# Performance work log

Measured on AMD Instinct MI355X. Metric: run time of the kernel, lower is better.

The kernel has to match this reference:

```python
import jax, jax.numpy as jnp
import numpy as np

B, N, T, H, F = 2, 1024, 12, 64, 1

def _diffuse(x, a):
    # x: (B,C,V), a: (B,W,V)  ->  (B,C,W)   (einsum 'ncvl,nwv->ncwl' with l=1)
    return jnp.einsum('bcv,bwv->bcw', x, a)

def _sconv(x, supports, order, include_self, W, b):
    feats = [x] if include_self else []
    for a in supports:
        x1 = _diffuse(x, a)
        feats.append(x1)
        for _ in range(order - 1):
            x1 = _diffuse(x1, a)
            feats.append(x1)
    z = jnp.concatenate(feats, axis=1)
    return jnp.einsum('bcn,oc->bon', z, W) + b[None, :, None]

def _lin(x, W, b):
    # Conv1d/Conv2d with kernel 1 == channel-wise linear
    return jnp.einsum('bcn,oc->bon', x, W) + b[None, :, None]

def setup_inputs():
    key = jax.random.key(0)
    ks = jax.random.split(key, 12)
    x = jax.random.normal(ks[0], (B, F, N, T), jnp.float32)
    mask = jax.random.randint(ks[1], (B, F, N, T), 0, 2, jnp.int32)
    adj = jax.random.uniform(ks[2], (2, B, N, N), jnp.float32)
    adj = adj / (adj.sum(-1, keepdims=True) + 1e-8)  # compute_support row-normalization
    cin_gate = 5 * (2 * F + H)  # (order*support_len+1)*(d_in+num_units) = 5*66
    s = 0.1
    Wr = s * jax.random.normal(ks[3], (H, cin_gate)); br = jnp.zeros((H,), jnp.float32)
    Wu = s * jax.random.normal(ks[4], (H, cin_gate)); bu = jnp.zeros((H,), jnp.float32)
    Wc = s * jax.random.normal(ks[5], (H, cin_gate)); bc = jnp.zeros((H,), jnp.float32)
    Wfs = s * jax.random.normal(ks[6], (F, H)); bfs = jnp.zeros((F,), jnp.float32)
    Wdin = s * jax.random.normal(ks[7], (H, 2 * F + H)); bdin = jnp.zeros((H,), jnp.float32)
    Wgc = s * jax.random.normal(ks[8], (H, 2 * H)); bgc = jnp.zeros((H,), jnp.float32)
    Wlout = s * jax.random.normal(ks[9], (H, 2 * H)); blout = jnp.zeros((H,), jnp.float32)
    Wro = s * jax.random.normal(ks[10], (F, 2 * H)); bro = jnp.zeros((F,), jnp.float32)
    prelu_a = 0.25 * jnp.ones((1,), jnp.float32)
    return dict(x=x, mask=mask, adj=adj, Wr=Wr, br=br, Wu=Wu, bu=bu, Wc=Wc, bc=bc,
                Wfs=Wfs, bfs=bfs, Wdin=Wdin, bdin=bdin, Wgc=Wgc, bgc=bgc,
                Wlout=Wlout, blout=blout, Wro=Wro, bro=bro, prelu_a=prelu_a)

def _gril(x, mask, adj, Wr, br, Wu, bu, Wc, bc, Wfs, bfs, Wdin, bdin,
          Wgc, bgc, Wlout, blout, Wro, bro, prelu_a):
    supports = [adj[0], adj[1]]
    h0 = jnp.zeros((x.shape[0], H, x.shape[2]), x.dtype)

    def step(h, inp):
        x_s, m_s = inp                  # (B,F,N), (B,F,N) int
        m_f = m_s.astype(x_s.dtype)
        m_b = m_s.astype(bool)
        # first stage prediction from hidden state
        xs1 = _lin(h, Wfs, bfs)
        x1 = jnp.where(m_b, x_s, xs1)
        # spatial decoder (order=1, no attention)
        x_in = _lin(jnp.concatenate([x1, m_f, h], axis=1), Wdin, bdin)
        out = _sconv(x_in, supports, 1, False, Wgc, bgc)
        out = _lin(jnp.concatenate([out, h], axis=1), Wlout, blout)
        out = jnp.where(out >= 0, out, prelu_a * out)   # PReLU
        repr_s = jnp.concatenate([out, h], axis=1)      # (B,2H,N)
        xs2 = _lin(repr_s, Wro, bro)
        x2 = jnp.where(m_b, x1, xs2)
        # GCGRU cell update (order=2 diffusion per gate)
        inp_c = jnp.concatenate([x2, m_f], axis=1)
        xh = jnp.concatenate([inp_c, h], axis=1)
        r = jax.nn.sigmoid(_sconv(xh, supports, 2, True, Wr, br))
        u = jax.nn.sigmoid(_sconv(xh, supports, 2, True, Wu, bu))
        xc = jnp.concatenate([inp_c, r * h], axis=1)
        c = jnp.tanh(_sconv(xc, supports, 2, True, Wc, bc))
        h_new = u * h + (1.0 - u) * c
        return h_new, (xs2, xs1, repr_s)

    xs = jnp.moveaxis(x, -1, 0)     # (T,B,F,N)
    ms = jnp.moveaxis(mask, -1, 0)
    _, (imps, preds, reprs) = jax.lax.scan(step, h0, (xs, ms))
    imputations = jnp.moveaxis(imps, 0, -1)       # (B,F,N,T)
    predictions = jnp.moveaxis(preds, 0, -1)      # (B,F,N,T)
    representations = jnp.moveaxis(reprs, 0, -1)  # (B,2H,N,T)
    return imputations, predictions, representations

def reference(x, mask, adj, Wr, br, Wu, bu, Wc, bc, Wfs, bfs, Wdin, bdin,
              Wgc, bgc, Wlout, blout, Wro, bro, prelu_a):
    return _gril(x, mask, adj, Wr, br, Wu, bu, Wc, bc, Wfs, bfs, Wdin, bdin,
                 Wgc, bgc, Wlout, blout, Wro, bro, prelu_a)
```

## Files before the change

### kernel.cpp

```cpp
#include <hip/hip_runtime.h>
#include <hip/hip_bf16.h>
#include <cstddef>

#define NN 1024
#define BB 2
#define TT 12
#define ZS 352

typedef __attribute__((ext_vector_type(8))) short short8;
typedef __attribute__((ext_vector_type(4))) short short4v;
typedef __attribute__((ext_vector_type(4))) float f32x4;
typedef __hip_bfloat16 bf16;

__device__ __forceinline__ float sigmoidf_(float v) { return 1.0f / (1.0f + expf(-v)); }
__device__ __forceinline__ short bf16s(float f) { bf16 h = __float2bfloat16(f); return *reinterpret_cast<short*>(&h); }

__device__ __forceinline__ float mapcol(const float* src, int c) {
    if (c < 64) return src[2 + c];
    if (c == 64) return src[0];
    if (c == 65) return src[1];
    if (c < 68 || c >= 340) return 0.f;
    const int d = c - 68, bk = d / 68, off = d % 68;
    if (off < 64) return src[66 + bk * 66 + 2 + off];
    if (off == 64) return src[66 + bk * 66];
    if (off == 65) return src[66 + bk * 66 + 1];
    return 0.f;
}

__global__ __launch_bounds__(256) void k_prep(
    const float* __restrict__ Wgc, const float* __restrict__ bgc,
    const float* __restrict__ Wdin, const float* __restrict__ bdin,
    const float* __restrict__ Wlout, const float* __restrict__ blout,
    const float* __restrict__ Wfs,
    const float* __restrict__ Wr, const float* __restrict__ Wu, const float* __restrict__ Wc,
    float* __restrict__ Wcomb, float* __restrict__ bcomb, float* __restrict__ blout2,
    bf16* __restrict__ Wpre, bf16* __restrict__ Wrub, bf16* __restrict__ Wcb,
    bf16* __restrict__ Wlb)
{
    const int idx = blockIdx.x * 256 + threadIdx.x;
    if (idx < 8448) {
        const int o = idx / 66, k = idx % 66;
        const float* g = Wgc + (size_t)(o & 63) * 128 + (o >> 6) * 64;
        float a = 0.f;
#pragma unroll 8
        for (int c = 0; c < 64; ++c) a += g[c] * Wdin[c * 66 + k];
        Wcomb[idx] = a;
    } else if (idx < 8576) {
        const int o = idx - 8448;
        const float* g = Wgc + (size_t)(o & 63) * 128 + (o >> 6) * 64;
        float a = 0.f;
#pragma unroll 8
        for (int c = 0; c < 64; ++c) a += g[c] * bdin[c];
        bcomb[o] = a;
    } else if (idx < 8640) {
        const int oc = idx - 8576;
        float a = blout[oc];
#pragma unroll 8
        for (int j = 0; j < 64; ++j) a += Wlout[(size_t)oc * 128 + j] * bgc[j];
        blout2[oc] = a;
    } else if (idx < 17856) {
        const int j = idx - 8640, r = j >> 6, k = j & 63;
        float v = 0.f;
        if (r == 0) v = Wfs[k];
        else if (r <= 128) {
            const int o = r - 1;
            const float* g = Wgc + (size_t)(o & 63) * 128 + (o >> 6) * 64;
#pragma unroll 8
            for (int c = 0; c < 64; ++c) v += g[c] * Wdin[c * 66 + 2 + k];
        }
        Wpre[j] = __float2bfloat16(v);
    } else if (idx < 62912) {
        const int j = idx - 17856, r = j / 352, c = j % 352;
        const float* src = (r < 64) ? (Wr + (size_t)r * 330) : (Wu + (size_t)(r - 64) * 330);
        Wrub[j] = __float2bfloat16(mapcol(src, c));
    } else if (idx < 85440) {
        const int j = idx - 62912, r = j / 352, c = j % 352;
        Wcb[j] = __float2bfloat16(mapcol(Wc + (size_t)r * 330, c));
    } else if (idx < 93632) {
        const int j = idx - 85440;
        Wlb[j] = __float2bfloat16(Wlout[j]);
    }
}

__global__ __launch_bounds__(256) void k_cvtT(const float* __restrict__ adj,
                                              bf16* __restrict__ adjb, bf16* __restrict__ adjtb)
{
    const int sb = blockIdx.z;
    const int r0 = blockIdx.y * 64, c0 = blockIdx.x * 64;
    const float* A = adj + ((size_t)sb << 20);
    __shared__ short tile[64][72];
    const int tr = threadIdx.x >> 4, tc = (threadIdx.x & 15) * 4;
#pragma unroll
    for (int i = 0; i < 4; ++i) {
        const int r = tr + i * 16;
        float4 v = *reinterpret_cast<const float4*>(&A[(size_t)(r0 + r) * NN + c0 + tc]);
        short4v o = { bf16s(v.x), bf16s(v.y), bf16s(v.z), bf16s(v.w) };
        *reinterpret_cast<short4v*>(&adjb[((size_t)sb << 20) + (size_t)(r0 + r) * NN + c0 + tc]) = o;
        tile[r][tc + 0] = o.x; tile[r][tc + 1] = o.y; tile[r][tc + 2] = o.z; tile[r][tc + 3] = o.w;
    }
    __syncthreads();
#pragma unroll
    for (int i = 0; i < 4; ++i) {
        const int v = tr + i * 16;
        short4v o = { tile[tc + 0][v], tile[tc + 1][v], tile[tc + 2][v], tile[tc + 3][v] };
        *reinterpret_cast<short4v*>(&adjtb[((size_t)sb << 20) + (size_t)(c0 + v) * NN + r0 + tc]) = o;
    }
}

__global__ __launch_bounds__(256) void k_a2(const bf16* __restrict__ adjb,
                                            const bf16* __restrict__ adjtb,
                                            bf16* __restrict__ adj2b)
{
    const int sb = blockIdx.z;
    const int wave = threadIdx.x >> 6, lane = threadIdx.x & 63;
    const int lr = lane & 15, lq = lane >> 4;
    const int v0 = blockIdx.x * 128 + wave * 32;
    const int w0 = blockIdx.y * 64;
    const bf16* AT = adjtb + ((size_t)sb << 20) + (size_t)(v0 + lr) * NN + lq * 8;
    const bf16* Ar = adjb + ((size_t)sb << 20) + (size_t)(w0 + lr) * NN + lq * 8;
    f32x4 acc[4][2];
#pragma unroll
    for (int m = 0; m < 4; ++m)
#pragma unroll
        for (int nb = 0; nb < 2; ++nb) acc[m][nb] = (f32x4){0.f, 0.f, 0.f, 0.f};
#pragma unroll 2
    for (int k0 = 0; k0 < NN; k0 += 32) {
        short8 bfr[2], af[4];
#pragma unroll
        for (int nb = 0; nb < 2; ++nb)
            bfr[nb] = *reinterpret_cast<const short8*>(AT + (size_t)nb * 16 * NN + k0);
#pragma unroll
        for (int m = 0; m < 4; ++m)
            af[m] = *reinterpret_cast<const short8*>(Ar + (size_t)m * 16 * NN + k0);
#pragma unroll
        for (int m = 0; m < 4; ++m)
#pragma unroll
            for (int nb = 0; nb < 2; ++nb)
                acc[m][nb] = __builtin_amdgcn_mfma_f32_16x16x32_bf16(af[m], bfr[nb], acc[m][nb], 0, 0, 0);
    }
    bf16* D = adj2b + ((size_t)sb << 20);
#pragma unroll
    for (int m = 0; m < 4; ++m)
#pragma unroll
        for (int nb = 0; nb < 2; ++nb)
#pragma unroll
            for (int q = 0; q < 4; ++q)
                D[(size_t)(w0 + m * 16 + lq * 4 + q) * NN + v0 + nb * 16 + lr] = __float2bfloat16(acc[m][nb][q]);
}

__global__ __launch_bounds__(64) void k_pre(
    const bf16* __restrict__ Wpre, const bf16* __restrict__ zT,
    const float* __restrict__ Wcomb, const float* __restrict__ bcomb,
    const float* __restrict__ bfsp,
    const float* __restrict__ x, const int* __restrict__ mask,
    bf16* __restrict__ yb, float* __restrict__ pred, int t)
{
    const int lane = threadIdx.x & 63, lr = lane & 15, lq = lane >> 4;
    const int p = blockIdx.x * 16 + lr;
    const bf16* B = zT + (size_t)p * ZS;
    f32x4 acc[9];
#pragma unroll
    for (int m = 0; m < 9; ++m) acc[m] = (f32x4){0.f, 0.f, 0.f, 0.f};
#pragma unroll
    for (int ks = 0; ks < 2; ++ks) {
        short8 bfr = *reinterpret_cast<const short8*>(B + ks * 32 + lq * 8);
#pragma unroll
        for (int m = 0; m < 9; ++m) {
            short8 af = *reinterpret_cast<const short8*>(Wpre + (size_t)(m * 16 + lr) * 64 + ks * 32 + lq * 8);
            acc[m] = __builtin_amdgcn_mfma_f32_16x16x32_bf16(af, bfr, acc[m], 0, 0, 0);
        }
    }
    const int b = p >> 10, n = p & (NN - 1);
    const size_t xi = (size_t)p * TT + t;
    const float xs1v = acc[0][0] + bfsp[0];
    const float xs1 = __shfl(xs1v, lr);
    const int mi = mask[xi];
    const float mf = (float)mi;
    const float x1 = mi ? x[xi] : xs1;
    if (lq == 0) pred[xi] = xs1;
#pragma unroll
    for (int m = 0; m < 9; ++m)
#pragma unroll
        for (int q = 0; q < 4; ++q) {
            const int o = m * 16 + lq * 4 + q - 1;
            if (o >= 0 && o < 128) {
                const float val = acc[m][q] + Wcomb[o * 66] * x1 + Wcomb[o * 66 + 1] * mf + bcomb[o];
                yb[(size_t)(b * 128 + o) * NN + n] = __float2bfloat16(val);
            }
        }
}

__global__ __launch_bounds__(256) void k_difA(
    const bf16* __restrict__ adjb, const bf16* __restrict__ adj2b,
    const bf16* __restrict__ yb, const bf16* __restrict__ zbi,
    const bf16* __restrict__ Wlb, const float* __restrict__ blout2,
    const float* __restrict__ prelu_a, const float* __restrict__ Wro,
    const float* __restrict__ bro, const float* __restrict__ x,
    const int* __restrict__ mask, const float* __restrict__ hTf,
    float* __restrict__ imp, float* __restrict__ repr,
    bf16* __restrict__ zb, bf16* __restrict__ zcb,
    bf16* __restrict__ zT, bf16* __restrict__ zcT, int t)
{
    const int wave = threadIdx.x >> 6, lane = threadIdx.x & 63;
    const int lr = lane & 15, lq = lane >> 4;
    const int n0 = blockIdx.x * 32;

    __shared__ f32x4 red[3][2][2][4][64];
    __shared__ short gh[32][136];
    __shared__ float hf[32][68];
    __shared__ float lo_sm[32][68];

    if (blockIdx.y >= 2) {
        const int i = blockIdx.y - 2;
        const int b = i & 1, s = (i >> 1) & 1, ord = i >> 2;
        const int sb = s * 2 + b;
        const bf16* M = (ord ? adj2b : adjb) + ((size_t)sb << 20);
        const bf16* A = M + (size_t)(n0 + lr) * NN + lq * 8;
        const bf16* Xp = zbi + ((size_t)(b * 66 + lr)) * NN + lq * 8;
        f32x4 acc[2][4];
#pragma unroll
        for (int nt = 0; nt < 2; ++nt)
#pragma unroll
            for (int m = 0; m < 4; ++m) acc[nt][m] = (f32x4){0.f, 0.f, 0.f, 0.f};
        const int vbeg = wave * 256;
#pragma unroll 2
        for (int it = 0; it < 8; ++it) {
            const int v0 = vbeg + it * 32;
            short8 bfr[2], af[4];
#pragma unroll
            for (int nt = 0; nt < 2; ++nt)
                bfr[nt] = *reinterpret_cast<const short8*>(A + (size_t)nt * 16 * NN + v0);
#pragma unroll
            for (int m = 0; m < 4; ++m)
                af[m] = *reinterpret_cast<const short8*>(Xp + (size_t)m * 16 * NN + v0);
#pragma unroll
            for (int nt = 0; nt < 2; ++nt)
#pragma unroll
                for (int m = 0; m < 4; ++m)
                    acc[nt][m] = __builtin_amdgcn_mfma_f32_16x16x32_bf16(af[m], bfr[nt], acc[nt][m], 0, 0, 0);
        }
        if (wave > 0) {
#pragma unroll
            for (int nt = 0; nt < 2; ++nt)
#pragma unroll
                for (int m = 0; m < 4; ++m) red[wave - 1][0][nt][m][lane] = acc[nt][m];
        }
        __syncthreads();
        if (wave == 0) {
#pragma unroll
            for (int nt = 0; nt < 2; ++nt) {
#pragma unroll
                for (int m = 0; m < 4; ++m)
                    acc[nt][m] += red[0][0][nt][m][lane] + red[1][0][nt][m][lane] + red[2][0][nt][m][lane];
                const int p = b * NN + n0 + nt * 16 + lr;
                bf16* dst = zT + (size_t)p * ZS + 68 + (s * 2 + ord) * 68;
#pragma unroll
                for (int m = 0; m < 4; ++m) {
                    short4v o = { bf16s(acc[nt][m][0]), bf16s(acc[nt][m][1]),
                                  bf16s(acc[nt][m][2]), bf16s(acc[nt][m][3]) };
                    *reinterpret_cast<short4v*>(dst + m * 16 + lq * 4) = o;
                }
            }
        }
        return;
    }

    const int b = blockIdx.y;
    f32x4 acc[2][2][4];
#pragma unroll
    for (int s = 0; s < 2; ++s)
#pragma unroll
        for (int nt = 0; nt < 2; ++nt)
#pragma unroll
            for (int m = 0; m < 4; ++m) acc[s][nt][m] = (f32x4){0.f, 0.f, 0.f, 0.f};
    {
        const int vbeg = wave * 256;
#pragma unroll 2
        for (int it = 0; it < 8; ++it) {
            const int v0 = vbeg + it * 32;
            short8 bfr[2][2], af[2][4];
#pragma unroll
            for (int s = 0; s < 2; ++s) {
                const bf16* M = adjb + ((size_t)(s * 2 + b) << 20);
#pragma unroll
                for (int nt = 0; nt < 2; ++nt)
                    bfr[s][nt] = *reinterpret_cast<const short8*>(M + (size_t)(n0 + nt * 16 + lr) * NN + v0 + lq * 8);
#pragma unroll
                for (int m = 0; m < 4; ++m)
                    af[s][m] = *reinterpret_cast<const short8*>(yb + (size_t)(b * 128 + s * 64 + m * 16 + lr) * NN + v0 + lq * 8);
            }
#pragma unroll
            for (int s = 0; s < 2; ++s)
#pragma unroll
                for (int nt = 0; nt < 2; ++nt)
#pragma unroll
                    for (int m = 0; m < 4; ++m)
                        acc[s][nt][m] = __builtin_amdgcn_mfma_f32_16x16x32_bf16(af[s][m], bfr[s][nt], acc[s][nt][m], 0, 0, 0);
        }
    }
    if (wave > 0) {
#pragma unroll
        for (int s = 0; s < 2; ++s)
#pragma unroll
            for (int nt = 0; nt < 2; ++nt)
#pragma unroll
                for (int m = 0; m < 4; ++m) red[wave - 1][s][nt][m][lane] = acc[s][nt][m];
    }
    if (wave == 1 || wave == 2) {
        const int nb = (wave - 1) * 16;
        for (int i = lane; i < 1024; i += 64) {
            const int node = nb + (i >> 6), oc = i & 63;
            const float hv = hTf[(size_t)(b * NN + n0 + node) * 64 + oc];
            hf[node][oc] = hv;
            gh[node][64 + oc] = bf16s(hv);
            repr[(((size_t)b * 128 + 64 + oc) * NN + (n0 + node)) * TT + t] = hv;
        }
    }
    __syncthreads();
    if (wave == 0) {
#pragma unroll
        for (int nt = 0; nt < 2; ++nt) {
#pragma unroll
            for (int m = 0; m < 4; ++m) {
                f32x4 g = acc[0][nt][m] + acc[1][nt][m];
#pragma unroll
                for (int w = 0; w < 3; ++w) g += red[w][0][nt][m][lane] + red[w][1][nt][m][lane];
                const int node = nt * 16 + lr;
#pragma unroll
                for (int q = 0; q < 4; ++q) gh[node][m * 16 + lq * 4 + q] = bf16s(g[q]);
            }
        }
    }
    __syncthreads();
    {
        f32x4 dacc[2];
#pragma unroll
        for (int nt = 0; nt < 2; ++nt) dacc[nt] = (f32x4){0.f, 0.f, 0.f, 0.f};
#pragma unroll
        for (int ks = 0; ks < 4; ++ks) {
            short8 af = *reinterpret_cast<const short8*>(Wlb + (size_t)(wave * 16 + lr) * 128 + ks * 32 + lq * 8);
#pragma unroll
            for (int nt = 0; nt < 2; ++nt) {
                short8 bfr = *reinterpret_cast<const short8*>(&gh[nt * 16 + lr][ks * 32 + lq * 8]);
                dacc[nt] = __builtin_amdgcn_mfma_f32_16x16x32_bf16(af, bfr, dacc[nt], 0, 0, 0);
            }
        }
        const float pa = prelu_a[0];
#pragma unroll
        for (int nt = 0; nt < 2; ++nt) {
            const int node = nt * 16 + lr;
#pragma unroll
            for (int q = 0; q < 4; ++q) {
                const int oc = wave * 16 + lq * 4 + q;
                float v = dacc[nt][q] + blout2[oc];
                v = (v >= 0.f) ? v : pa * v;
                repr[(((size_t)b * 128 + oc) * NN + (n0 + node)) * TT + t] = v;
                lo_sm[node][oc] = v;
            }
        }
    }
    __syncthreads();
    {
        const int node = threadIdx.x >> 3, sub = threadIdx.x & 7;
        float s = 0.f;
#pragma unroll
        for (int j = sub * 8; j < sub * 8 + 8; ++j)
            s += Wro[j] * lo_sm[node][j] + Wro[64 + j] * hf[node][j];
        s += __shfl_xor(s, 1); s += __shfl_xor(s, 2); s += __shfl_xor(s, 4);
        if (sub == 0) {
            const float xs2 = s + bro[0];
            const int n = n0 + node;
            const int p = b * NN + n;
            const size_t xi = (size_t)p * TT + t;
            imp[xi] = xs2;
            const int mi = mask[xi];
            const float x2 = mi ? x[xi] : xs2;
            const bf16 x2b = __float2bfloat16(x2);
            const bf16 mb = __float2bfloat16((float)mi);
            zb[((size_t)b * 66 + 64) * NN + n] = x2b;
            zb[((size_t)b * 66 + 65) * NN + n] = mb;
            zcb[((size_t)b * 66 + 64) * NN + n] = x2b;
            zcb[((size_t)b * 66 + 65) * NN + n] = mb;
            zT[(size_t)p * ZS + 64] = x2b; zT[(size_t)p * ZS + 65] = mb;
            zcT[(size_t)p * ZS + 64] = x2b; zcT[(size_t)p * ZS + 65] = mb;
        }
    }
}

__global__ __launch_bounds__(256) void k_difN(
    const bf16* __restrict__ adjb, const bf16* __restrict__ adj2b,
    const bf16* __restrict__ zcb, float* __restrict__ gcT_unused,
    bf16* __restrict__ zcT)
{
    const int i = blockIdx.y;
    const int b = i & 1, s = (i >> 1) & 1, ord = i >> 2;
    const int wave = threadIdx.x >> 6, lane = threadIdx.x & 63;
    const int lr = lane & 15, lq = lane >> 4;
    const int n0 = blockIdx.x * 32;
    const int sb = s * 2 + b;
    const bf16* M = (ord ? adj2b : adjb) + ((size_t)sb << 20);
    const bf16* A = M + (size_t)(n0 + lr) * NN + lq * 8;
    const bf16* Xp = zcb + ((size_t)(b * 66 + lr)) * NN + lq * 8;

    f32x4 acc[2][4];
#pragma unroll
    for (int nt = 0; nt < 2; ++nt)
#pragma unroll
        for (int m = 0; m < 4; ++m) acc[nt][m] = (f32x4){0.f, 0.f, 0.f, 0.f};
    const int vbeg = wave * 256;
#pragma unroll 2
    for (int it = 0; it < 8; ++it) {
        const int v0 = vbeg + it * 32;
        short8 bfr[2], af[4];
#pragma unroll
        for (int nt = 0; nt < 2; ++nt)
            bfr[nt] = *reinterpret_cast<const short8*>(A + (size_t)nt * 16 * NN + v0);
#pragma unroll
        for (int m = 0; m < 4; ++m)
            af[m] = *reinterpret_cast<const short8*>(Xp + (size_t)m * 16 * NN + v0);
#pragma unroll
        for (int nt = 0; nt < 2; ++nt)
#pragma unroll
            for (int m = 0; m < 4; ++m)
                acc[nt][m] = __builtin_amdgcn_mfma_f32_16x16x32_bf16(af[m], bfr[nt], acc[nt][m], 0, 0, 0);
    }
    __shared__ f32x4 red[3][2][4][64];
    if (wave > 0) {
#pragma unroll
        for (int nt = 0; nt < 2; ++nt)
#pragma unroll
            for (int m = 0; m < 4; ++m) red[wave - 1][nt][m][lane] = acc[nt][m];
    }
    __syncthreads();
    if (wave == 0) {
#pragma unroll
        for (int nt = 0; nt < 2; ++nt) {
#pragma unroll
            for (int m = 0; m < 4; ++m)
                acc[nt][m] += red[0][nt][m][lane] + red[1][nt][m][lane] + red[2][nt][m][lane];
            const int p = b * NN + n0 + nt * 16 + lr;
            bf16* dst = zcT + (size_t)p * ZS + 68 + (s * 2 + ord) * 68;
#pragma unroll
            for (int m = 0; m < 4; ++m) {
                short4v o = { bf16s(acc[nt][m][0]), bf16s(acc[nt][m][1]),
                              bf16s(acc[nt][m][2]), bf16s(acc[nt][m][3]) };
                *reinterpret_cast<short4v*>(dst + m * 16 + lq * 4) = o;
            }
        }
    }
}

__global__ __launch_bounds__(256) void k_dif2(
    const bf16* __restrict__ adjb, const bf16* __restrict__ adj2b,
    const bf16* __restrict__ zb, bf16* __restrict__ zT, bf16* __restrict__ zcT)
{
    const int i = blockIdx.y;
    const int b = i & 1, s = (i >> 1) & 1, ord = i >> 2;
    const int sb = s * 2 + b;
    const int wave = threadIdx.x >> 6, lane = threadIdx.x & 63;
    const int lr = lane & 15, lq = lane >> 4;
    const int n0 = blockIdx.x * 16;
    const bf16* M = (ord ? adj2b : adjb) + ((size_t)sb << 20);
    const bf16* A = M + (size_t)(n0 + lr) * NN + lq * 8;
    const bf16* Xp = zb + ((size_t)(b * 66 + 64) + lr) * NN + lq * 8;

    f32x4 acc = (f32x4){0.f, 0.f, 0.f, 0.f};
    const short8 zsh = {0, 0, 0, 0, 0, 0, 0, 0};
    const int vbeg = wave * 256;
#pragma unroll 4
    for (int i2 = 0; i2 < 8; ++i2) {
        const int v0 = vbeg + i2 * 32;
        short8 bfr = *reinterpret_cast<const short8*>(A + v0);
        short8 af = (lr < 2) ? *reinterpret_cast<const short8*>(Xp + v0) : zsh;
        acc = __builtin_amdgcn_mfma_f32_16x16x32_bf16(af, bfr, acc, 0, 0, 0);
    }
    __shared__ f32x4 red2[3][64];
    if (wave > 0) red2[wave - 1][lane] = acc;
    __syncthreads();
    if (wave == 0 && lq == 0) {
        acc += red2[0][lane] + red2[1][lane] + red2[2][lane];
        const int p = b * NN + n0 + lr;
        const size_t off = (size_t)p * ZS + 68 + (s * 2 + ord) * 68 + 64;
#pragma unroll
        for (int q = 0; q < 2; ++q) {
            const bf16 v = __float2bfloat16(acc[q]);
            zT[off + q] = v; zcT[off + q] = v;
        }
    }
}

__global__ __launch_bounds__(128) void k_gates(
    const bf16* __restrict__ Wrub, const bf16* __restrict__ zT,
    const float* __restrict__ br, const float* __restrict__ bu,
    const float* __restrict__ hTf,
    float* __restrict__ uT, bf16* __restrict__ zcb, bf16* __restrict__ zcT)
{
    const int wave = threadIdx.x >> 6, lane = threadIdx.x & 63;
    const int lr = lane & 15, lq = lane >> 4;
    const int p = blockIdx.x * 16 + lr;
    const bf16* B = zT + (size_t)p * ZS;
    const bf16* WA = Wrub + (size_t)wave * 64 * ZS;
    f32x4 acc[4];
#pragma unroll
    for (int m = 0; m < 4; ++m) acc[m] = (f32x4){0.f, 0.f, 0.f, 0.f};
#pragma unroll 2
    for (int ks = 0; ks < 11; ++ks) {
        short8 bfr = *reinterpret_cast<const short8*>(B + ks * 32 + lq * 8);
#pragma unroll
        for (int m = 0; m < 4; ++m) {
            short8 af = *reinterpret_cast<const short8*>(WA + (size_t)(m * 16 + lr) * ZS + ks * 32 + lq * 8);
            acc[m] = __builtin_amdgcn_mfma_f32_16x16x32_bf16(af, bfr, acc[m], 0, 0, 0);
        }
    }
    const int b = p >> 10, n = p & (NN - 1);
    if (wave == 0) {
#pragma unroll
        for (int m = 0; m < 4; ++m) {
            short4v rq;
#pragma unroll
            for (int q = 0; q < 4; ++q) {
                const int oc = m * 16 + lq * 4 + q;
                const float rv = sigmoidf_(acc[m][q] + br[oc]);
                const float rh = rv * hTf[(size_t)p * 64 + oc];
                rq[q] = bf16s(rh);
                zcb[((size_t)b * 66 + oc) * NN + n] = __float2bfloat16(rh);
            }
            *reinterpret_cast<short4v*>(&zcT[(size_t)p * ZS + m * 16 + lq * 4]) = rq;
        }
    } else {
#pragma unroll
        for (int m = 0; m < 4; ++m) {
            f32x4 uq;
#pragma unroll
            for (int q = 0; q < 4; ++q) {
                const int oc = m * 16 + lq * 4 + q;
                uq[q] = sigmoidf_(acc[m][q] + bu[oc]);
            }
            *reinterpret_cast<f32x4*>(&uT[(size_t)p * 64 + m * 16 + lq * 4]) = uq;
        }
    }
}

__global__ __launch_bounds__(128) void k_cellpre(
    const bf16* __restrict__ Wcb, const bf16* __restrict__ zcT,
    const float* __restrict__ bc, const float* __restrict__ uT,
    float* __restrict__ hTf, bf16* __restrict__ zT, bf16* __restrict__ zb,
    const bf16* __restrict__ Wpre, const float* __restrict__ Wcomb,
    const float* __restrict__ bcomb, const float* __restrict__ bfsp,
    const float* __restrict__ x, const int* __restrict__ mask,
    bf16* __restrict__ yb, float* __restrict__ pred, int tn)
{
    const int wave = threadIdx.x >> 6, lane = threadIdx.x & 63;
    const int lr = lane & 15, lq = lane >> 4;
    const int p = blockIdx.x * 16 + lr;
    const int b = p >> 10, n = p & (NN - 1);
    __shared__ short hsm[16][72];
    __shared__ float xs1s[16];

    {
        const bf16* B = zcT + (size_t)p * ZS;
        f32x4 acc[2];
#pragma unroll
        for (int mm = 0; mm < 2; ++mm) acc[mm] = (f32x4){0.f, 0.f, 0.f, 0.f};
#pragma unroll 2
        for (int ks = 0; ks < 11; ++ks) {
            short8 bfr = *reinterpret_cast<const short8*>(B + ks * 32 + lq * 8);
#pragma unroll
            for (int mm = 0; mm < 2; ++mm) {
                const int m = wave * 2 + mm;
                short8 af = *reinterpret_cast<const short8*>(Wcb + (size_t)(m * 16 + lr) * ZS + ks * 32 + lq * 8);
                acc[mm] = __builtin_amdgcn_mfma_f32_16x16x32_bf16(af, bfr, acc[mm], 0, 0, 0);
            }
        }
#pragma unroll
        for (int mm = 0; mm < 2; ++mm) {
            const int m = wave * 2 + mm;
            f32x4 hq;
            short4v hb;
#pragma unroll
            for (int q = 0; q < 4; ++q) {
                const int oc = m * 16 + lq * 4 + q;
                const float cv = tanhf(acc[mm][q] + bc[oc]);
                const float uv = uT[(size_t)p * 64 + oc];
                const float ho = hTf[(size_t)p * 64 + oc];
                const float hn = uv * ho + (1.f - uv) * cv;
                hq[q] = hn;
                hb[q] = bf16s(hn);
                zb[((size_t)b * 66 + oc) * NN + n] = __float2bfloat16(hn);
            }
            *reinterpret_cast<f32x4*>(&hTf[(size_t)p * 64 + m * 16 + lq * 4]) = hq;
            *reinterpret_cast<short4v*>(&zT[(size_t)p * ZS + m * 16 + lq * 4]) = hb;
            *reinterpret_cast<short4v*>(&hsm[lr][m * 16 + lq * 4]) = hb;
        }
    }
    __syncthreads();

    {
        const int MB = wave ? 4 : 5;
        f32x4 acc[5];
#pragma unroll
        for (int m = 0; m < 5; ++m) acc[m] = (f32x4){0.f, 0.f, 0.f, 0.f};
#pragma unroll
        for (int ks = 0; ks < 2; ++ks) {
            short8 bfr = *reinterpret_cast<const short8*>(&hsm[lr][ks * 32 + lq * 8]);
#pragma unroll
            for (int m = 0; m < 5; ++m) {
                if (m < MB) {
                    const int mm = wave ? 5 + m : m;
                    short8 af = *reinterpret_cast<const short8*>(Wpre + (size_t)(mm * 16 + lr) * 64 + ks * 32 + lq * 8);
                    acc[m] = __builtin_amdgcn_mfma_f32_16x16x32_bf16(af, bfr, acc[m], 0, 0, 0);
                }
            }
        }
        if (wave == 0 && lq == 0) xs1s[lr] = acc[0][0] + bfsp[0];
        __syncthreads();
        const float xs1 = xs1s[lr];
        const size_t xi = (size_t)p * TT + tn;
        const int mi = mask[xi];
        const float mf = (float)mi;
        const float x1 = mi ? x[xi] : xs1;
        if (wave == 0 && lq == 0) pred[xi] = xs1;
#pragma unroll
        for (int m = 0; m < 5; ++m) {
            if (m < MB) {
                const int mm = wave ? 5 + m : m;
#pragma unroll
                for (int q = 0; q < 4; ++q) {
                    const int o = mm * 16 + lq * 4 + q - 1;
                    if (o >= 0 && o < 128) {
                        const float val = acc[m][q] + Wcomb[o * 66] * x1 + Wcomb[o * 66 + 1] * mf + bcomb[o];
                        yb[(size_t)(b * 128 + o) * NN + n] = __float2bfloat16(val);
                    }
                }
            }
        }
    }
}

extern "C" void kernel_launch(void* const* d_in, const int* in_sizes, int n_in,
                              void* d_out, int out_size, void* d_ws, size_t ws_size,
                              hipStream_t stream)
{
    const float* x     = (const float*)d_in[0];
    const int*   mask  = (const int*)  d_in[1];
    const float* adj   = (const float*)d_in[2];
    const float* Wr    = (const float*)d_in[3];
    const float* br    = (const float*)d_in[4];
    const float* Wu    = (const float*)d_in[5];
    const float* bu    = (const float*)d_in[6];
    const float* Wc    = (const float*)d_in[7];
    const float* bc    = (const float*)d_in[8];
    const float* Wfs   = (const float*)d_in[9];
    const float* bfs   = (const float*)d_in[10];
    const float* Wdin  = (const float*)d_in[11];
    const float* bdin  = (const float*)d_in[12];
    const float* Wgc   = (const float*)d_in[13];
    const float* bgc   = (const float*)d_in[14];
    const float* Wlout = (const float*)d_in[15];
    const float* blout = (const float*)d_in[16];
    const float* Wro   = (const float*)d_in[17];
    const float* bro   = (const float*)d_in[18];
    const float* pa    = (const float*)d_in[19];

    float* ws = (float*)d_ws;
    float* Wcomb  = ws + 0;
    float* bcomb  = ws + 8448;
    float* blout2 = ws + 8576;
    float* uT     = ws + 272832;
    float* hTf    = ws + 403904;
    bf16* bfp   = (bf16*)(ws + 534976);
    bf16* zb    = bfp + 0;
    bf16* zcb   = bfp + 135168;
    bf16* zT    = bfp + 270336;
    bf16* zcT   = bfp + 991232;
    bf16* adjb  = bfp + 1712128;
    bf16* adjtb = bfp + 5906432;
    bf16* adj2b = bfp + 10100736;
    bf16* yb    = bfp + 14295040;
    bf16* Wpre  = bfp + 14557184;
    bf16* Wrub  = bfp + 14566400;
    bf16* Wcb   = bfp + 14611456;
    bf16* Wlb   = bfp + 14633984;

    float* imp  = (float*)d_out;
    float* pred = imp + (size_t)BB * NN * TT;
    float* repr = imp + (size_t)2 * BB * NN * TT;

    hipMemsetAsync(hTf, 0, 131072 * 4 + (size_t)1712128 * 2, stream);
    hipLaunchKernelGGL(k_prep, dim3(366), dim3(256), 0, stream,
                       Wgc, bgc, Wdin, bdin, Wlout, blout, Wfs, Wr, Wu, Wc,
                       Wcomb, bcomb, blout2, Wpre, Wrub, Wcb, Wlb);
    hipLaunchKernelGGL(k_cvtT, dim3(16, 16, 4), dim3(256), 0, stream, adj, adjb, adjtb);
    hipLaunchKernelGGL(k_a2, dim3(8, 16, 4), dim3(256), 0, stream, adjb, adjtb, adj2b);

    hipLaunchKernelGGL(k_pre, dim3(128), dim3(64), 0, stream,
                       Wpre, zT, Wcomb, bcomb, bfs, x, mask, yb, pred, 0);

    for (int t = 0; t < TT; ++t) {
        const int ny = (t < TT - 1) ? 10 : 2;
        hipLaunchKernelGGL(k_difA, dim3(32, ny), dim3(256), 0, stream,
                           adjb, adj2b, yb, zb, Wlb, blout2, pa, Wro, bro, x, mask,
                           hTf, imp, repr, zb, zcb, zT, zcT, t);
        if (t < TT - 1) {
            hipLaunchKernelGGL(k_dif2, dim3(64, 8), dim3(256), 0, stream,
                               adjb, adj2b, zb, zT, zcT);
            hipLaunchKernelGGL(k_gates, dim3(128), dim3(128), 0, stream,
                               Wrub, zT, br, bu, hTf, uT, zcb, zcT);
            hipLaunchKernelGGL(k_difN, dim3(32, 8), dim3(256), 0, stream,
                               adjb, adj2b, zcb, (float*)nullptr, zcT);
            hipLaunchKernelGGL(k_cellpre, dim3(128), dim3(128), 0, stream,
                               Wcb, zcT, bc, uT, hTf, zT, zb,
                               Wpre, Wcomb, bcomb, bfs, x, mask, yb, pred, t + 1);
        }
    }
}
```

Measured before the change: 705.0 us.

## Fuse input-channel diffusion into gates kernel and apply it as fp32 rank-8 correction

Removes the separate k_dif2 launch that diffused the two input channels (x2, mask) and wrote them into zT/zcT. The gates kernel now runs those diffusions on two extra waves alongside the MFMA gate GEMM. The results are applied as an fp32 rank-8 correction using weights split out of Wr/Wu/Wc, and are stored to a buffer so the cell kernel can reuse them. This saves one launch per timestep and keeps those columns in fp32, at the cost of a larger block in k_gates and extra scalar correction math.

```diff
diff --git a/kernel.cpp b/kernel.cpp
--- a/kernel.cpp
+++ b/kernel.cpp
@@ -15,15 +15,13 @@
 __device__ __forceinline__ float sigmoidf_(float v) { return 1.0f / (1.0f + expf(-v)); }
 __device__ __forceinline__ short bf16s(float f) { bf16 h = __float2bfloat16(f); return *reinterpret_cast<short*>(&h); }
 
-__device__ __forceinline__ float mapcol(const float* src, int c) {
+__device__ __forceinline__ float mapcolz(const float* src, int c) {
     if (c < 64) return src[2 + c];
     if (c == 64) return src[0];
     if (c == 65) return src[1];
     if (c < 68 || c >= 340) return 0.f;
     const int d = c - 68, bk = d / 68, off = d % 68;
     if (off < 64) return src[66 + bk * 66 + 2 + off];
-    if (off == 64) return src[66 + bk * 66];
-    if (off == 65) return src[66 + bk * 66 + 1];
     return 0.f;
 }
 
@@ -35,7 +33,7 @@
     const float* __restrict__ Wr, const float* __restrict__ Wu, const float* __restrict__ Wc,
     float* __restrict__ Wcomb, float* __restrict__ bcomb, float* __restrict__ blout2,
     bf16* __restrict__ Wpre, bf16* __restrict__ Wrub, bf16* __restrict__ Wcb,
-    bf16* __restrict__ Wlb)
+    bf16* __restrict__ Wlb, float* __restrict__ Wrux, float* __restrict__ Wcx)
 {
     const int idx = blockIdx.x * 256 + threadIdx.x;
     if (idx < 8448) {
@@ -72,13 +70,20 @@
     } else if (idx < 62912) {
         const int j = idx - 17856, r = j / 352, c = j % 352;
         const float* src = (r < 64) ? (Wr + (size_t)r * 330) : (Wu + (size_t)(r - 64) * 330);
-        Wrub[j] = __float2bfloat16(mapcol(src, c));
+        Wrub[j] = __float2bfloat16(mapcolz(src, c));
     } else if (idx < 85440) {
         const int j = idx - 62912, r = j / 352, c = j % 352;
-        Wcb[j] = __float2bfloat16(mapcol(Wc + (size_t)r * 330, c));
+        Wcb[j] = __float2bfloat16(mapcolz(Wc + (size_t)r * 330, c));
     } else if (idx < 93632) {
         const int j = idx - 85440;
         Wlb[j] = __float2bfloat16(Wlout[j]);
+    } else if (idx < 94656) {
+        const int j2 = idx - 93632, r = j2 >> 3, j = j2 & 7;
+        const float* src = (r < 64) ? (Wr + (size_t)r * 330) : (Wu + (size_t)(r - 64) * 330);
+        Wrux[j2] = src[66 + (j >> 1) * 66 + (j & 1)];
+    } else if (idx < 95168) {
+        const int j2 = idx - 94656, r = j2 >> 3, j = j2 & 7;
+        Wcx[j2] = Wc[(size_t)r * 330 + 66 + (j >> 1) * 66 + (j & 1)];
     }
 }
 
@@ -379,8 +384,6 @@
             const bf16 mb = __float2bfloat16((float)mi);
             zb[((size_t)b * 66 + 64) * NN + n] = x2b;
             zb[((size_t)b * 66 + 65) * NN + n] = mb;
-            zcb[((size_t)b * 66 + 64) * NN + n] = x2b;
-            zcb[((size_t)b * 66 + 65) * NN + n] = mb;
             zT[(size_t)p * ZS + 64] = x2b; zT[(size_t)p * ZS + 65] = mb;
             zcT[(size_t)p * ZS + 64] = x2b; zcT[(size_t)p * ZS + 65] = mb;
         }
@@ -389,8 +392,7 @@
 
 __global__ __launch_bounds__(256) void k_difN(
     const bf16* __restrict__ adjb, const bf16* __restrict__ adj2b,
-    const bf16* __restrict__ zcb, float* __restrict__ gcT_unused,
-    bf16* __restrict__ zcT)
+    const bf16* __restrict__ zcb, bf16* __restrict__ zcT)
 {
     const int i = blockIdx.y;
     const int b = i & 1, s = (i >> 1) & 1, ord = i >> 2;
@@ -450,93 +452,100 @@
     }
 }
 
-__global__ __launch_bounds__(256) void k_dif2(
-    const bf16* __restrict__ adjb, const bf16* __restrict__ adj2b,
-    const bf16* __restrict__ zb, bf16* __restrict__ zT, bf16* __restrict__ zcT)
-{
-    const int i = blockIdx.y;
-    const int b = i & 1, s = (i >> 1) & 1, ord = i >> 2;
-    const int sb = s * 2 + b;
-    const int wave = threadIdx.x >> 6, lane = threadIdx.x & 63;
-    const int lr = lane & 15, lq = lane >> 4;
-    const int n0 = blockIdx.x * 16;
-    const bf16* M = (ord ? adj2b : adjb) + ((size_t)sb << 20);
-    const bf16* A = M + (size_t)(n0 + lr) * NN + lq * 8;
-    const bf16* Xp = zb + ((size_t)(b * 66 + 64) + lr) * NN + lq * 8;
-
-    f32x4 acc = (f32x4){0.f, 0.f, 0.f, 0.f};
-    const short8 zsh = {0, 0, 0, 0, 0, 0, 0, 0};
-    const int vbeg = wave * 256;
-#pragma unroll 4
-    for (int i2 = 0; i2 < 8; ++i2) {
-        const int v0 = vbeg + i2 * 32;
-        short8 bfr = *reinterpret_cast<const short8*>(A + v0);
-        short8 af = (lr < 2) ? *reinterpret_cast<const short8*>(Xp + v0) : zsh;
-        acc = __builtin_amdgcn_mfma_f32_16x16x32_bf16(af, bfr, acc, 0, 0, 0);
-    }
-    __shared__ f32x4 red2[3][64];
-    if (wave > 0) red2[wave - 1][lane] = acc;
-    __syncthreads();
-    if (wave == 0 && lq == 0) {
-        acc += red2[0][lane] + red2[1][lane] + red2[2][lane];
-        const int p = b * NN + n0 + lr;
-        const size_t off = (size_t)p * ZS + 68 + (s * 2 + ord) * 68 + 64;
-#pragma unroll
-        for (int q = 0; q < 2; ++q) {
-            const bf16 v = __float2bfloat16(acc[q]);
-            zT[off + q] = v; zcT[off + q] = v;
-        }
-    }
-}
-
-__global__ __launch_bounds__(128) void k_gates(
+__global__ __launch_bounds__(256) void k_gates(
     const bf16* __restrict__ Wrub, const bf16* __restrict__ zT,
     const float* __restrict__ br, const float* __restrict__ bu,
     const float* __restrict__ hTf,
+    const bf16* __restrict__ adjb, const bf16* __restrict__ adj2b,
+    const bf16* __restrict__ zb, const float* __restrict__ Wrux,
+    float* __restrict__ xdg,
     float* __restrict__ uT, bf16* __restrict__ zcb, bf16* __restrict__ zcT)
 {
     const int wave = threadIdx.x >> 6, lane = threadIdx.x & 63;
     const int lr = lane & 15, lq = lane >> 4;
     const int p = blockIdx.x * 16 + lr;
-    const bf16* B = zT + (size_t)p * ZS;
-    const bf16* WA = Wrub + (size_t)wave * 64 * ZS;
+    const int b = blockIdx.x >> 6;
+    const int n0 = (blockIdx.x & 63) * 16;
+    __shared__ float xds[8][16];
+    __shared__ float wxs[128][8];
+
     f32x4 acc[4];
 #pragma unroll
     for (int m = 0; m < 4; ++m) acc[m] = (f32x4){0.f, 0.f, 0.f, 0.f};
+
+    if (wave < 2) {
+#pragma unroll
+        for (int j = 0; j < 8; ++j) wxs[threadIdx.x][j] = Wrux[threadIdx.x * 8 + j];
+        const bf16* B = zT + (size_t)p * ZS;
+        const bf16* WA = Wrub + (size_t)wave * 64 * ZS;
 #pragma unroll 2
-    for (int ks = 0; ks < 11; ++ks) {
-        short8 bfr = *reinterpret_cast<const short8*>(B + ks * 32 + lq * 8);
-#pragma unroll
-        for (int m = 0; m < 4; ++m) {
-            short8 af = *reinterpret_cast<const short8*>(WA + (size_t)(m * 16 + lr) * ZS + ks * 32 + lq * 8);
-            acc[m] = __builtin_amdgcn_mfma_f32_16x16x32_bf16(af, bfr, acc[m], 0, 0, 0);
-        }
-    }
-    const int b = p >> 10, n = p & (NN - 1);
-    if (wave == 0) {
-#pragma unroll
-        for (int m = 0; m < 4; ++m) {
-            short4v rq;
-#pragma unroll
-            for (int q = 0; q < 4; ++q) {
-                const int oc = m * 16 + lq * 4 + q;
-                const float rv = sigmoidf_(acc[m][q] + br[oc]);
-                const float rh = rv * hTf[(size_t)p * 64 + oc];
-                rq[q] = bf16s(rh);
-                zcb[((size_t)b * 66 + oc) * NN + n] = __float2bfloat16(rh);
-            }
-            *reinterpret_cast<short4v*>(&zcT[(size_t)p * ZS + m * 16 + lq * 4]) = rq;
+        for (int ks = 0; ks < 11; ++ks) {
+            short8 bfr = *reinterpret_cast<const short8*>(B + ks * 32 + lq * 8);
+#pragma unroll
+            for (int m = 0; m < 4; ++m) {
+                short8 af = *reinterpret_cast<const short8*>(WA + (size_t)(m * 16 + lr) * ZS + ks * 32 + lq * 8);
+                acc[m] = __builtin_amdgcn_mfma_f32_16x16x32_bf16(af, bfr, acc[m], 0, 0, 0);
+            }
         }
     } else {
-#pragma unroll
-        for (int m = 0; m < 4; ++m) {
-            f32x4 uq;
-#pragma unroll
-            for (int q = 0; q < 4; ++q) {
-                const int oc = m * 16 + lq * 4 + q;
-                uq[q] = sigmoidf_(acc[m][q] + bu[oc]);
-            }
-            *reinterpret_cast<f32x4*>(&uT[(size_t)p * 64 + m * 16 + lq * 4]) = uq;
+        const int w2 = wave - 2;
+        const int j0 = w2 * 2;
+        const int s0 = j0 >> 1, o0 = j0 & 1;
+        const int s1 = (j0 + 1) >> 1, o1 = (j0 + 1) & 1;
+        const bf16* Xp = zb + (size_t)(b * 66 + 64 + lr) * NN + lq * 8;
+        const bf16* M0 = (o0 ? adj2b : adjb) + ((size_t)(s0 * 2 + b) << 20) + (size_t)(n0 + lr) * NN + lq * 8;
+        const bf16* M1 = (o1 ? adj2b : adjb) + ((size_t)(s1 * 2 + b) << 20) + (size_t)(n0 + lr) * NN + lq * 8;
+        f32x4 a0 = (f32x4){0.f, 0.f, 0.f, 0.f}, a1 = (f32x4){0.f, 0.f, 0.f, 0.f};
+        const short8 zsh = {0, 0, 0, 0, 0, 0, 0, 0};
+#pragma unroll 4
+        for (int v0 = 0; v0 < NN; v0 += 32) {
+            short8 af = (lr < 2) ? *reinterpret_cast<const short8*>(Xp + v0) : zsh;
+            a0 = __builtin_amdgcn_mfma_f32_16x16x32_bf16(af, *reinterpret_cast<const short8*>(M0 + v0), a0, 0, 0, 0);
+            a1 = __builtin_amdgcn_mfma_f32_16x16x32_bf16(af, *reinterpret_cast<const short8*>(M1 + v0), a1, 0, 0, 0);
+        }
+        if (lq == 0) {
+            xds[j0 * 2 + 0][lr] = a0[0]; xds[j0 * 2 + 1][lr] = a0[1];
+            xds[j0 * 2 + 2][lr] = a1[0]; xds[j0 * 2 + 3][lr] = a1[1];
+            float* xg = xdg + ((size_t)b * 8) * NN + n0 + lr;
+            xg[(size_t)(j0 * 2 + 0) * NN] = a0[0]; xg[(size_t)(j0 * 2 + 1) * NN] = a0[1];
+            xg[(size_t)(j0 * 2 + 2) * NN] = a1[0]; xg[(size_t)(j0 * 2 + 3) * NN] = a1[1];
+        }
+    }
+    __syncthreads();
+
+    if (wave < 2) {
+        const int n = p & (NN - 1);
+        if (wave == 0) {
+#pragma unroll
+            for (int m = 0; m < 4; ++m) {
+                short4v rq;
+#pragma unroll
+                for (int q = 0; q < 4; ++q) {
+                    const int oc = m * 16 + lq * 4 + q;
+                    float corr = 0.f;
+#pragma unroll
+                    for (int j = 0; j < 8; ++j) corr += wxs[oc][j] * xds[j][lr];
+                    const float rv = sigmoidf_(acc[m][q] + corr + br[oc]);
+                    const float rh = rv * hTf[(size_t)p * 64 + oc];
+                    rq[q] = bf16s(rh);
+                    zcb[((size_t)b * 66 + oc) * NN + n] = __float2bfloat16(rh);
+                }
+                *reinterpret_cast<short4v*>(&zcT[(size_t)p * ZS + m * 16 + lq * 4]) = rq;
+            }
+        } else {
+#pragma unroll
+            for (int m = 0; m < 4; ++m) {
+                f32x4 uq;
+#pragma unroll
+                for (int q = 0; q < 4; ++q) {
+                    const int oc = m * 16 + lq * 4 + q;
+                    float corr = 0.f;
+#pragma unroll
+                    for (int j = 0; j < 8; ++j) corr += wxs[64 + oc][j] * xds[j][lr];
+                    uq[q] = sigmoidf_(acc[m][q] + corr + bu[oc]);
+                }
+                *reinterpret_cast<f32x4*>(&uT[(size_t)p * 64 + m * 16 + lq * 4]) = uq;
+            }
         }
     }
 }
@@ -548,14 +557,27 @@
     const bf16* __restrict__ Wpre, const float* __restrict__ Wcomb,
     const float* __restrict__ bcomb, const float* __restrict__ bfsp,
     const float* __restrict__ x, const int* __restrict__ mask,
+    const float* __restrict__ xdg, const float* __restrict__ Wcx,
     bf16* __restrict__ yb, float* __restrict__ pred, int tn)
 {
     const int wave = threadIdx.x >> 6, lane = threadIdx.x & 63;
     const int lr = lane & 15, lq = lane >> 4;
     const int p = blockIdx.x * 16 + lr;
-    const int b = p >> 10, n = p & (NN - 1);
+    const int b = blockIdx.x >> 6;
+    const int n0 = (blockIdx.x & 63) * 16;
+    const int n = p & (NN - 1);
     __shared__ short hsm[16][72];
     __shared__ float xs1s[16];
+    __shared__ float xds2[8][16];
+    __shared__ float wcxs[64][8];
+
+    {
+        const int ti = threadIdx.x;
+        xds2[ti >> 4][ti & 15] = xdg[((size_t)b * 8 + (ti >> 4)) * NN + n0 + (ti & 15)];
+#pragma unroll
+        for (int i = ti; i < 512; i += 128) wcxs[i >> 3][i & 7] = Wcx[i];
+    }
+    __syncthreads();
 
     {
         const bf16* B = zcT + (size_t)p * ZS;
@@ -580,7 +602,10 @@
 #pragma unroll
             for (int q = 0; q < 4; ++q) {
                 const int oc = m * 16 + lq * 4 + q;
-                const float cv = tanhf(acc[mm][q] + bc[oc]);
+                float corr = 0.f;
+#pragma unroll
+                for (int j = 0; j < 8; ++j) corr += wcxs[oc][j] * xds2[j][lr];
+                const float cv = tanhf(acc[mm][q] + corr + bc[oc]);
                 const float uv = uT[(size_t)p * 64 + oc];
                 const float ho = hTf[(size_t)p * 64 + oc];
                 const float hn = uv * ho + (1.f - uv) * cv;
@@ -666,6 +691,9 @@
     float* Wcomb  = ws + 0;
     float* bcomb  = ws + 8448;
     float* blout2 = ws + 8576;
+    float* Wrux   = ws + 8640;
+    float* Wcx    = ws + 9664;
+    float* xdg    = ws + 10176;
     float* uT     = ws + 272832;
     float* hTf    = ws + 403904;
     bf16* bfp   = (bf16*)(ws + 534976);
@@ -687,9 +715,9 @@
     float* repr = imp + (size_t)2 * BB * NN * TT;
 
     hipMemsetAsync(hTf, 0, 131072 * 4 + (size_t)1712128 * 2, stream);
-    hipLaunchKernelGGL(k_prep, dim3(366), dim3(256), 0, stream,
+    hipLaunchKernelGGL(k_prep, dim3(372), dim3(256), 0, stream,
                        Wgc, bgc, Wdin, bdin, Wlout, blout, Wfs, Wr, Wu, Wc,
-                       Wcomb, bcomb, blout2, Wpre, Wrub, Wcb, Wlb);
+                       Wcomb, bcomb, blout2, Wpre, Wrub, Wcb, Wlb, Wrux, Wcx);
     hipLaunchKernelGGL(k_cvtT, dim3(16, 16, 4), dim3(256), 0, stream, adj, adjb, adjtb);
     hipLaunchKernelGGL(k_a2, dim3(8, 16, 4), dim3(256), 0, stream, adjb, adjtb, adj2b);
 
@@ -702,15 +730,15 @@
                            adjb, adj2b, yb, zb, Wlb, blout2, pa, Wro, bro, x, mask,
                            hTf, imp, repr, zb, zcb, zT, zcT, t);
         if (t < TT - 1) {
-            hipLaunchKernelGGL(k_dif2, dim3(64, 8), dim3(256), 0, stream,
-                               adjb, adj2b, zb, zT, zcT);
-            hipLaunchKernelGGL(k_gates, dim3(128), dim3(128), 0, stream,
-                               Wrub, zT, br, bu, hTf, uT, zcb, zcT);
+            hipLaunchKernelGGL(k_gates, dim3(128), dim3(256), 0, stream,
+                               Wrub, zT, br, bu, hTf, adjb, adj2b, zb, Wrux, xdg,
+                               uT, zcb, zcT);
             hipLaunchKernelGGL(k_difN, dim3(32, 8), dim3(256), 0, stream,
-                               adjb, adj2b, zcb, (float*)nullptr, zcT);
+                               adjb, adj2b, zcb, zcT);
             hipLaunchKernelGGL(k_cellpre, dim3(128), dim3(128), 0, stream,
                                Wcb, zcT, bc, uT, hTf, zT, zb,
-                               Wpre, Wcomb, bcomb, bfs, x, mask, yb, pred, t + 1);
-        }
-    }
-}
+                               Wpre, Wcomb, bcomb, bfs, x, mask, xdg, Wcx,
+                               yb, pred, t + 1);
+        }
+    }
+}
```

Result: slower. 769.2 us (+9.1%).

## Prefetch MFMA operands and skip first-step diffusion work when hidden state is zero

Applied to the files above, without the earlier changes.

Adds register double-buffering to the adj² GEMM and the k_difN diffusion loop, so the next K-slice loads are issued before the current MFMAs run and global-load latency can be hidden. At t=0 it also skips k_difN and shrinks the k_difA grid, apparently relying on the hidden state (and so r*h) being zero at the first step. It stops writing the x2/mask rows into zcb inside k_difA. If those zcb rows or the skipped diffusion outputs are read anywhere, results could change, and the prefetch adds register pressure.

```diff
diff --git a/kernel.cpp b/kernel.cpp
--- a/kernel.cpp
+++ b/kernel.cpp
@@ -123,20 +123,36 @@
     for (int m = 0; m < 4; ++m)
 #pragma unroll
         for (int nb = 0; nb < 2; ++nb) acc[m][nb] = (f32x4){0.f, 0.f, 0.f, 0.f};
-#pragma unroll 2
+
+    short8 bfr[2], af[4];
+#pragma unroll
+    for (int nb = 0; nb < 2; ++nb) bfr[nb] = *reinterpret_cast<const short8*>(AT + (size_t)nb * 16 * NN);
+#pragma unroll
+    for (int m = 0; m < 4; ++m) af[m] = *reinterpret_cast<const short8*>(Ar + (size_t)m * 16 * NN);
+
+#pragma unroll 4
     for (int k0 = 0; k0 < NN; k0 += 32) {
-        short8 bfr[2], af[4];
-#pragma unroll
-        for (int nb = 0; nb < 2; ++nb)
-            bfr[nb] = *reinterpret_cast<const short8*>(AT + (size_t)nb * 16 * NN + k0);
-#pragma unroll
-        for (int m = 0; m < 4; ++m)
-            af[m] = *reinterpret_cast<const short8*>(Ar + (size_t)m * 16 * NN + k0);
+        short8 bfr_n[2], af_n[4];
+        const int kn = k0 + 32;
+        if (kn < NN) {
+#pragma unroll
+            for (int nb = 0; nb < 2; ++nb)
+                bfr_n[nb] = *reinterpret_cast<const short8*>(AT + (size_t)nb * 16 * NN + kn);
+#pragma unroll
+            for (int m = 0; m < 4; ++m)
+                af_n[m] = *reinterpret_cast<const short8*>(Ar + (size_t)m * 16 * NN + kn);
+        }
 #pragma unroll
         for (int m = 0; m < 4; ++m)
 #pragma unroll
             for (int nb = 0; nb < 2; ++nb)
                 acc[m][nb] = __builtin_amdgcn_mfma_f32_16x16x32_bf16(af[m], bfr[nb], acc[m][nb], 0, 0, 0);
+        if (kn < NN) {
+#pragma unroll
+            for (int nb = 0; nb < 2; ++nb) bfr[nb] = bfr_n[nb];
+#pragma unroll
+            for (int m = 0; m < 4; ++m) af[m] = af_n[m];
+        }
     }
     bf16* D = adj2b + ((size_t)sb << 20);
 #pragma unroll
@@ -379,8 +395,6 @@
             const bf16 mb = __float2bfloat16((float)mi);
             zb[((size_t)b * 66 + 64) * NN + n] = x2b;
             zb[((size_t)b * 66 + 65) * NN + n] = mb;
-            zcb[((size_t)b * 66 + 64) * NN + n] = x2b;
-            zcb[((size_t)b * 66 + 65) * NN + n] = mb;
             zT[(size_t)p * ZS + 64] = x2b; zT[(size_t)p * ZS + 65] = mb;
             zcT[(size_t)p * ZS + 64] = x2b; zcT[(size_t)p * ZS + 65] = mb;
         }
@@ -389,8 +403,7 @@
 
 __global__ __launch_bounds__(256) void k_difN(
     const bf16* __restrict__ adjb, const bf16* __restrict__ adj2b,
-    const bf16* __restrict__ zcb, float* __restrict__ gcT_unused,
-    bf16* __restrict__ zcT)
+    const bf16* __restrict__ zcb, bf16* __restrict__ zcT)
 {
     const int i = blockIdx.y;
     const int b = i & 1, s = (i >> 1) & 1, ord = i >> 2;
@@ -408,21 +421,38 @@
 #pragma unroll
         for (int m = 0; m < 4; ++m) acc[nt][m] = (f32x4){0.f, 0.f, 0.f, 0.f};
     const int vbeg = wave * 256;
+
+    short8 bfr[2], af[4];
+#pragma unroll
+    for (int nt = 0; nt < 2; ++nt)
+        bfr[nt] = *reinterpret_cast<const short8*>(A + (size_t)nt * 16 * NN + vbeg);
+#pragma unroll
+    for (int m = 0; m < 4; ++m)
+        af[m] = *reinterpret_cast<const short8*>(Xp + (size_t)m * 16 * NN + vbeg);
+
 #pragma unroll 2
     for (int it = 0; it < 8; ++it) {
-        const int v0 = vbeg + it * 32;
-        short8 bfr[2], af[4];
-#pragma unroll
-        for (int nt = 0; nt < 2; ++nt)
-            bfr[nt] = *reinterpret_cast<const short8*>(A + (size_t)nt * 16 * NN + v0);
-#pragma unroll
-        for (int m = 0; m < 4; ++m)
-            af[m] = *reinterpret_cast<const short8*>(Xp + (size_t)m * 16 * NN + v0);
+        const int vn = vbeg + it * 32 + 32;
+        short8 bfr_n[2], af_n[4];
+        if (it < 7) {
+#pragma unroll
+            for (int nt = 0; nt < 2; ++nt)
+                bfr_n[nt] = *reinterpret_cast<const short8*>(A + (size_t)nt * 16 * NN + vn);
+#pragma unroll
+            for (int m = 0; m < 4; ++m)
+                af_n[m] = *reinterpret_cast<const short8*>(Xp + (size_t)m * 16 * NN + vn);
+        }
 #pragma unroll
         for (int nt = 0; nt < 2; ++nt)
 #pragma unroll
             for (int m = 0; m < 4; ++m)
                 acc[nt][m] = __builtin_amdgcn_mfma_f32_16x16x32_bf16(af[m], bfr[nt], acc[nt][m], 0, 0, 0);
+        if (it < 7) {
+#pragma unroll
+            for (int nt = 0; nt < 2; ++nt) bfr[nt] = bfr_n[nt];
+#pragma unroll
+            for (int m = 0; m < 4; ++m) af[m] = af_n[m];
+        }
     }
     __shared__ f32x4 red[3][2][4][64];
     if (wave > 0) {
@@ -697,7 +727,7 @@
                        Wpre, zT, Wcomb, bcomb, bfs, x, mask, yb, pred, 0);
 
     for (int t = 0; t < TT; ++t) {
-        const int ny = (t < TT - 1) ? 10 : 2;
+        const int ny = (t > 0 && t < TT - 1) ? 10 : 2;
         hipLaunchKernelGGL(k_difA, dim3(32, ny), dim3(256), 0, stream,
                            adjb, adj2b, yb, zb, Wlb, blout2, pa, Wro, bro, x, mask,
                            hTf, imp, repr, zb, zcb, zT, zcT, t);
@@ -706,8 +736,10 @@
                                adjb, adj2b, zb, zT, zcT);
             hipLaunchKernelGGL(k_gates, dim3(128), dim3(128), 0, stream,
                                Wrub, zT, br, bu, hTf, uT, zcb, zcT);
-            hipLaunchKernelGGL(k_difN, dim3(32, 8), dim3(256), 0, stream,
-                               adjb, adj2b, zcb, (float*)nullptr, zcT);
+            if (t > 0) {
+                hipLaunchKernelGGL(k_difN, dim3(32, 8), dim3(256), 0, stream,
+                                   adjb, adj2b, zcb, zcT);
+            }
             hipLaunchKernelGGL(k_cellpre, dim3(128), dim3(128), 0, stream,
                                Wcb, zcT, bc, uT, hTf, zT, zb,
                                Wpre, Wcomb, bcomb, bfs, x, mask, yb, pred, t + 1);
```

Result: no change. 695.5 us (-1.3%).
